# Performance work log

Measured on AMD Instinct MI355X. Metric: run time of the kernel, lower is better.

The kernel has to match this reference:

```python
import jax, jax.numpy as jnp
import numpy as np

B, N, IN_DIM = 64, 4096, 128
D = 128          # slot_size
S = 7            # num_slots
ITERS = 3
HID = 256        # mlp_hdim
EPS = 1e-8       # renorm epsilon
LN_EPS = 1e-5    # torch LayerNorm default


def _ln(x, g, b):
    m = jnp.mean(x, axis=-1, keepdims=True)
    v = jnp.mean((x - m) ** 2, axis=-1, keepdims=True)
    return (x - m) * jax.lax.rsqrt(v + LN_EPS) * g + b


def setup_inputs() -> dict:
    key = jax.random.key(0)
    ks = jax.random.split(key, 16)
    s = 0.02
    return {
        "x": jax.random.normal(ks[0], (B, N, IN_DIM), jnp.float32),
        "noise": jax.random.normal(ks[1], (B, S, D), jnp.float32),
        "Wq": jax.random.normal(ks[2], (D, D), jnp.float32) * s,
        "Wk": jax.random.normal(ks[3], (D, IN_DIM), jnp.float32) * s,
        "Wv": jax.random.normal(ks[4], (D, IN_DIM), jnp.float32) * s,
        "ln_in_g": jnp.ones((IN_DIM,), jnp.float32),
        "ln_in_b": jnp.zeros((IN_DIM,), jnp.float32),
        "ln_slots_g": jnp.ones((D,), jnp.float32),
        "ln_slots_b": jnp.zeros((D,), jnp.float32),
        "ln_mlp_g": jnp.ones((D,), jnp.float32),
        "ln_mlp_b": jnp.zeros((D,), jnp.float32),
        "W_ih": jax.random.normal(ks[5], (3 * D, D), jnp.float32) * s,
        "W_hh": jax.random.normal(ks[6], (3 * D, D), jnp.float32) * s,
        "b_ih": jnp.zeros((3 * D,), jnp.float32),
        "b_hh": jnp.zeros((3 * D,), jnp.float32),
        "W1": jax.random.normal(ks[7], (HID, D), jnp.float32) * s,
        "b1": jnp.zeros((HID,), jnp.float32),
        "W2": jax.random.normal(ks[8], (D, HID), jnp.float32) * s,
        "b2": jnp.zeros((D,), jnp.float32),
        "mu": jax.random.normal(ks[9], (1, 1, D), jnp.float32) * s,
        "logsigma": jax.random.normal(ks[10], (1, D), jnp.float32) * s,
    }


def reference(x, noise, Wq, Wk, Wv, ln_in_g, ln_in_b, ln_slots_g, ln_slots_b,
              ln_mlp_g, ln_mlp_b, W_ih, W_hh, b_ih, b_hh, W1, b1, W2, b2,
              mu, logsigma):
    xn = _ln(x, ln_in_g, ln_in_b)              # (B,N,IN)
    k = xn @ Wk.T                              # (B,N,D)
    v = xn @ Wv.T                              # (B,N,D)

    scale = jax.nn.softplus(logsigma)[None] + 1e-5   # (1,1,D)
    slots = mu + scale * noise                 # rsample, (B,S,D)

    def gru(u, h):
        gx = u @ W_ih.T + b_ih                 # (B*S, 3D)
        gh = h @ W_hh.T + b_hh
        xr, xz, xn_ = jnp.split(gx, 3, axis=-1)
        hr, hz, hn = jnp.split(gh, 3, axis=-1)
        r = jax.nn.sigmoid(xr + hr)
        z = jax.nn.sigmoid(xz + hz)
        n = jnp.tanh(xn_ + r * hn)
        return (1.0 - z) * n + z * h

    inv_sqrt_d = D ** -0.5
    for _ in range(ITERS):
        slots_prev = slots
        sn = _ln(slots, ln_slots_g, ln_slots_b)
        q = sn @ Wq.T                          # (B,S,D)
        scores = inv_sqrt_d * jnp.einsum('bnd,bsd->bns', k, q)
        attn = jax.nn.softmax(scores, axis=-1)           # over slots
        attn = attn + EPS
        attn = attn / jnp.sum(attn, axis=1, keepdims=True)  # renorm over inputs
        updates = jnp.einsum('bns,bnd->bsd', attn, v)    # (B,S,D)
        h = gru(updates.reshape(-1, D), slots_prev.reshape(-1, D))
        slots = h.reshape(x.shape[0], S, D)
        slots = _ln(slots, ln_mlp_g, ln_mlp_b)
        slots = slots + (jax.nn.relu(slots @ W1.T + b1) @ W2.T + b2)
    return slots
```

## Files before the change

kernel.cpp:

```cpp
#include <hip/hip_runtime.h>
#include <hip/hip_bf16.h>
#include <stdint.h>

#define B_ 64
#define N_ 4096
#define D_ 128
#define S_ 7
#define EPS_ 1e-8f
#define LN_EPS_ 1e-5f
#define SC_INV 0.08838834764831843f

typedef float  f32x4  __attribute__((ext_vector_type(4)));
typedef __bf16 bf16x8 __attribute__((ext_vector_type(8)));

#define WIH_OFF 0
#define WHH_OFF 49152
#define W1_OFF  98304
#define W2_OFF  131072
#define WQ_OFF  163840
#define WKT_OFF 180224
#define WV_OFF  196608
#define WBF_TOT 212992

__device__ __forceinline__ uint16_t f2bfbits(float f) {
    uint32_t x = __float_as_uint(f);
    return (uint16_t)((x + 0x7fffu + ((x >> 16) & 1u)) >> 16);
}
__device__ __forceinline__ uint32_t pk2(float a, float b) {
    return (uint32_t)f2bfbits(a) | ((uint32_t)f2bfbits(b) << 16);
}

__global__ __launch_bounds__(256) void k_init_prep(
    const float* __restrict__ noise, const float* __restrict__ Wk,
    const float* __restrict__ mu, const float* __restrict__ logsigma,
    const float* __restrict__ Wq, const float* __restrict__ lsg,
    const float* __restrict__ lsb,
    const float* __restrict__ Wih, const float* __restrict__ Whh,
    const float* __restrict__ W1, const float* __restrict__ W2,
    const float* __restrict__ Wv,
    float* __restrict__ slots, uint16_t* __restrict__ kqbf,
    uint16_t* __restrict__ wbf,
    const float* __restrict__ x, const float* __restrict__ lng,
    const float* __restrict__ lnb, uint16_t* __restrict__ xn) {
    const int t = threadIdx.x;
    if (blockIdx.x < 448) {
        __shared__ float sn[128], qr[128];
        __shared__ float red[2];
        const int tid = blockIdx.x * 256 + t;
        const int row = blockIdx.x;
        const int b = row / 7, s = row - b * 7;
        bool act = t < 128;
        float v = 0.f;
        if (act) {
            float sc = log1pf(__expf(logsigma[t])) + 1e-5f;
            v = mu[t] + sc * noise[row * 128 + t];
            slots[row * 128 + t] = v;
        }
        float sv = act ? v : 0.f;
        #pragma unroll
        for (int m = 1; m < 64; m <<= 1) sv += __shfl_xor(sv, m);
        if (act && (t & 63) == 0) red[t >> 6] = sv;
        __syncthreads();
        float mean = (red[0] + red[1]) * (1.0f / 128.0f);
        __syncthreads();
        float dv = act ? (v - mean) : 0.f;
        float sq = dv * dv;
        #pragma unroll
        for (int m = 1; m < 64; m <<= 1) sq += __shfl_xor(sq, m);
        if (act && (t & 63) == 0) red[t >> 6] = sq;
        __syncthreads();
        float var = (red[0] + red[1]) * (1.0f / 128.0f);
        if (act) sn[t] = dv * rsqrtf(var + LN_EPS_) * lsg[t] + lsb[t];
        __syncthreads();
        if (act) {
            const float4* wr = (const float4*)(Wq + t * 128);
            float acc = 0.f;
            #pragma unroll 8
            for (int j = 0; j < 32; ++j) {
                float4 w = wr[j];
                float4 s4 = *(const float4*)(sn + 4 * j);
                acc += w.x * s4.x + w.y * s4.y + w.z * s4.z + w.w * s4.w;
            }
            qr[t] = acc;
        }
        __syncthreads();
        if (act) {
            float kq = 0.f;
            #pragma unroll 8
            for (int o = 0; o < 128; ++o) kq += qr[o] * Wk[o * 128 + t];
            int elem = (t >> 5) * 512 + (s + 16 * ((t >> 3) & 3)) * 8 + (t & 7);
            kqbf[b * 2048 + elem] = f2bfbits(kq * SC_INV);
        }
        if (tid < 73728) {
            int bb = tid / 1152, rem = tid - bb * 1152;
            int sp = 7 + (rem >> 7), d = rem & 127;
            int elem = (d >> 5) * 512 + (sp + 16 * ((d >> 3) & 3)) * 8 + (d & 7);
            kqbf[bb * 2048 + elem] = 0;
        }
        for (int e = tid; e < WBF_TOT; e += 448 * 256) {
            const float* W; int C, el, mode = 0;
            if (e < WHH_OFF)      { W = Wih; C = 128; el = e; }
            else if (e < W1_OFF)  { W = Whh; C = 128; el = e - WHH_OFF; }
            else if (e < W2_OFF)  { W = W1;  C = 128; el = e - W1_OFF; }
            else if (e < WQ_OFF)  { W = W2;  C = 256; el = e - W2_OFF; }
            else if (e < WKT_OFF) { W = Wq;  C = 128; el = e - WQ_OFF; }
            else if (e < WV_OFF)  { W = Wk;  C = 128; el = e - WKT_OFF; mode = 1; }
            else                  { W = Wv;  C = 128; el = e - WV_OFF; }
            int tile = el >> 9, within = el & 511;
            int lp = within >> 3, j = within & 7;
            int lm_ = lp & 15, qd_ = lp >> 4;
            float w;
            if (!mode) {
                int ktN = C >> 5, ot = tile / ktN, kt = tile - ot * ktN;
                w = W[(ot * 16 + lm_) * C + kt * 32 + qd_ * 8 + j];
            } else {
                int dt = tile >> 2, kt = tile & 3;
                w = W[(kt * 32 + qd_ * 8 + j) * 128 + dt * 16 + lm_];
            }
            wbf[e] = f2bfbits(w);
        }
        return;
    }
    const int pid = blockIdx.x - 448;
    const int wv = t >> 6, lane = t & 63;
    const int lm = lane & 15, hi = lane >> 4;
    const long row = (long)pid * 64 + wv * 16 + lm;
    const long ntile = (long)pid * 4 + wv;
    const float* xp = x + row * 128 + hi * 8;
    f32x4 xa[4][2];
    #pragma unroll
    for (int k0 = 0; k0 < 4; ++k0) {
        xa[k0][0] = *(const f32x4*)(xp + k0 * 32);
        xa[k0][1] = *(const f32x4*)(xp + k0 * 32 + 4);
    }
    float s = 0.f, sq = 0.f;
    #pragma unroll
    for (int k0 = 0; k0 < 4; ++k0)
        #pragma unroll
        for (int c = 0; c < 2; ++c)
            #pragma unroll
            for (int r = 0; r < 4; ++r) { float v = xa[k0][c][r]; s += v; sq += v * v; }
    s  += __shfl_xor(s, 16);  s  += __shfl_xor(s, 32);
    sq += __shfl_xor(sq, 16); sq += __shfl_xor(sq, 32);
    float mean = s * (1.0f / 128.0f);
    float var  = sq * (1.0f / 128.0f) - mean * mean;
    float rs   = rsqrtf(var + LN_EPS_);
    #pragma unroll
    for (int k0 = 0; k0 < 4; ++k0) {
        f32x4 g0 = *(const f32x4*)(lng + k0 * 32 + hi * 8);
        f32x4 g1 = *(const f32x4*)(lng + k0 * 32 + hi * 8 + 4);
        f32x4 b0 = *(const f32x4*)(lnb + k0 * 32 + hi * 8);
        f32x4 b1 = *(const f32x4*)(lnb + k0 * 32 + hi * 8 + 4);
        float v[8];
        #pragma unroll
        for (int r = 0; r < 4; ++r) {
            v[r]     = (xa[k0][0][r] - mean) * rs * g0[r] + b0[r];
            v[4 + r] = (xa[k0][1][r] - mean) * rs * g1[r] + b1[r];
        }
        uint4 st;
        st.x = pk2(v[0], v[1]); st.y = pk2(v[2], v[3]);
        st.z = pk2(v[4], v[5]); st.w = pk2(v[6], v[7]);
        *(uint4*)(xn + (ntile * 4 + k0) * 512 + lane * 8) = st;
    }
}

__global__ __launch_bounds__(256, 4) void k_attn(
    const uint16_t* __restrict__ xn, const uint16_t* __restrict__ kqbf,
    float* __restrict__ upart, float* __restrict__ cpart) {
    __shared__ __align__(16) uint16_t stage[4][32 * 132];
    __shared__ __align__(16) uint16_t als[4][16 * 36];
    __shared__ float bsum[4][8];
    const int t = threadIdx.x, wv = t >> 6, lane = t & 63;
    const int lm = lane & 15, qd = lane >> 4;
    const int b = blockIdx.x >> 4, chunk = blockIdx.x & 15;
    const int ntb = b * 256 + chunk * 16 + wv * 4;
    const int sbase = qd * 4;

    bf16x8 kqf[4];
    #pragma unroll
    for (int k0 = 0; k0 < 4; ++k0)
        kqf[k0] = *(const bf16x8*)(kqbf + b * 2048 + k0 * 512 + lane * 8);

    bf16x8 xfs[2][2][4];
    #pragma unroll
    for (int sub = 0; sub < 2; ++sub)
        #pragma unroll
        for (int nt = 0; nt < 2; ++nt)
            #pragma unroll
            for (int k0 = 0; k0 < 4; ++k0)
                xfs[sub][nt][k0] = *(const bf16x8*)(xn +
                    ((long)(ntb + sub * 2 + nt) * 4 + k0) * 512 + lane * 8);

    uint16_t* xw = stage[wv];
    float* prt = (float*)stage[wv];
    uint16_t* aw = als[wv];
    f32x4 uacc[8];
    #pragma unroll
    for (int i = 0; i < 8; ++i) uacc[i] = (f32x4){0.f, 0.f, 0.f, 0.f};
    f32x4 csl = {0.f, 0.f, 0.f, 0.f};

    #pragma unroll
    for (int sub = 0; sub < 2; ++sub) {
        #pragma unroll
        for (int nt = 0; nt < 2; ++nt)
            #pragma unroll
            for (int k0 = 0; k0 < 4; ++k0) {
                int base = (nt * 16 + lm) * 132 + k0 * 32 + qd * 8;
                const uint2* src = (const uint2*)&xfs[sub][nt][k0];
                *(uint2*)(xw + base)     = src[0];
                *(uint2*)(xw + base + 4) = src[1];
            }
        f32x4 sc[2];
        #pragma unroll
        for (int nt = 0; nt < 2; ++nt) {
            f32x4 acc = {0.f, 0.f, 0.f, 0.f};
            #pragma unroll
            for (int k0 = 0; k0 < 4; ++k0)
                acc = __builtin_amdgcn_mfma_f32_16x16x32_bf16(kqf[k0], xfs[sub][nt][k0], acc, 0, 0, 0);
            sc[nt] = acc;
        }
        #pragma unroll
        for (int nt = 0; nt < 2; ++nt) {
            float mx = -1e30f;
            #pragma unroll
            for (int r = 0; r < 4; ++r)
                if (sbase + r < 7) mx = fmaxf(mx, sc[nt][r]);
            mx = fmaxf(mx, __shfl_xor(mx, 16));
            mx = fmaxf(mx, __shfl_xor(mx, 32));
            float e[4], tot = 0.f;
            #pragma unroll
            for (int r = 0; r < 4; ++r) {
                e[r] = (sbase + r < 7) ? __expf(sc[nt][r] - mx) : 0.f;
                tot += e[r];
            }
            tot += __shfl_xor(tot, 16);
            tot += __shfl_xor(tot, 32);
            float inv = 1.0f / tot;
            #pragma unroll
            for (int r = 0; r < 4; ++r) {
                float a_ = (sbase + r < 7) ? e[r] * inv + EPS_ : 0.f;
                csl[r] += a_;
                aw[(sbase + r) * 36 + nt * 16 + lm] = f2bfbits(a_);
            }
        }
        union { uint2 u[2]; bf16x8 v; } cva;
        cva.u[0] = *(const uint2*)(aw + lm * 36 + qd * 8);
        cva.u[1] = *(const uint2*)(aw + lm * 36 + qd * 8 + 4);
        bf16x8 afr = cva.v;
        #pragma unroll
        for (int dt = 0; dt < 8; ++dt) {
            bf16x8 bfr;
            #pragma unroll
            for (int j = 0; j < 8; ++j)
                bfr[j] = ((const __bf16*)xw)[(qd * 8 + j) * 132 + dt * 16 + lm];
            uacc[dt] = __builtin_amdgcn_mfma_f32_16x16x32_bf16(afr, bfr, uacc[dt], 0, 0, 0);
        }
    }
    #pragma unroll
    for (int m = 1; m < 16; m <<= 1) {
        csl[0] += __shfl_xor(csl[0], m);
        csl[1] += __shfl_xor(csl[1], m);
        csl[2] += __shfl_xor(csl[2], m);
        csl[3] += __shfl_xor(csl[3], m);
    }
    if (lm == 0) {
        #pragma unroll
        for (int r = 0; r < 4; ++r) {
            int s = sbase + r;
            if (s < 7) bsum[wv][s] = csl[r];
        }
    }
    #pragma unroll
    for (int dt = 0; dt < 8; ++dt)
        #pragma unroll
        for (int r = 0; r < 4; ++r) {
            int s = sbase + r;
            if (s < 7) prt[s * 132 + dt * 16 + lm] = uacc[dt][r];
        }
    __syncthreads();
    if (t < 128) {
        const float* p0 = (const float*)stage[0];
        const float* p1 = (const float*)stage[1];
        const float* p2 = (const float*)stage[2];
        const float* p3 = (const float*)stage[3];
        #pragma unroll
        for (int s = 0; s < 7; ++s) {
            int o = s * 132 + t;
            upart[((b * 16 + chunk) * 7 + s) * 128 + t] = p0[o] + p1[o] + p2[o] + p3[o];
        }
    }
    if (t < 7)
        cpart[(b * 16 + chunk) * 7 + t] = bsum[0][t] + bsum[1][t] + bsum[2][t] + bsum[3][t];
}

__global__ __launch_bounds__(256) void k_fused(
    const float* __restrict__ upart, const float* __restrict__ cpart,
    float* __restrict__ slots, const uint16_t* __restrict__ wbf,
    const float* __restrict__ bih, const float* __restrict__ bhh,
    const float* __restrict__ gm, const float* __restrict__ bm,
    const float* __restrict__ b1, const float* __restrict__ b2,
    const float* __restrict__ lsg, const float* __restrict__ lsb,
    uint16_t* __restrict__ kqbf, float* __restrict__ dst, int hasq) {
    __shared__ float uf[16][132];
    __shared__ float hf[16][132];
    __shared__ float slf[16][132];
    __shared__ float hidl[16][264];
    __shared__ float glg[7][776];
    __shared__ float csl[7];
    const int b = blockIdx.x;
    const int t = threadIdx.x, wv = t >> 6, lane = t & 63;
    const int lm = lane & 15, qd = lane >> 4;

    if (t < 7) {
        float c = 0.f;
        #pragma unroll
        for (int i = 0; i < 16; ++i) c += cpart[(b * 16 + i) * 7 + t];
        csl[t] = c;
    }
    for (int idx = t; idx < 896; idx += 256) {
        int s = idx >> 7, d = idx & 127;
        float acc = 0.f;
        #pragma unroll
        for (int i = 0; i < 16; ++i) acc += upart[((b * 16 + i) * 7 + s) * 128 + d];
        slf[s][d] = acc;
        hf[s][d] = slots[(b * 7 + s) * 128 + d];
    }
    __syncthreads();

    {
        bf16x8 apb[4];
        #pragma unroll
        for (int k0 = 0; k0 < 4; ++k0)
            #pragma unroll
            for (int j = 0; j < 8; ++j) apb[k0][j] = (__bf16)slf[lm][k0 * 32 + qd * 8 + j];
        #pragma unroll
        for (int i = 0; i < 2; ++i) {
            int dt = wv * 2 + i;
            f32x4 acc = {0.f, 0.f, 0.f, 0.f};
            #pragma unroll
            for (int k0 = 0; k0 < 4; ++k0) {
                bf16x8 bf = *(const bf16x8*)(wbf + WV_OFF + ((dt * 4 + k0) << 9) + lane * 8);
                acc = __builtin_amdgcn_mfma_f32_16x16x32_bf16(apb[k0], bf, acc, 0, 0, 0);
            }
            #pragma unroll
            for (int r = 0; r < 4; ++r) {
                int s = qd * 4 + r;
                if (s < 7) uf[s][dt * 16 + lm] = acc[r] / csl[s];
            }
        }
    }
    __syncthreads();

    bf16x8 au[4], ah[4];
    #pragma unroll
    for (int k0 = 0; k0 < 4; ++k0)
        #pragma unroll
        for (int j = 0; j < 8; ++j) {
            au[k0][j] = (__bf16)uf[lm][k0 * 32 + qd * 8 + j];
            ah[k0][j] = (__bf16)hf[lm][k0 * 32 + qd * 8 + j];
        }
    {
        const int ih = (wv < 2);
        const uint16_t* W = wbf + (ih ? WIH_OFF : WHH_OFF);
        const int base = ih ? 0 : 384;
        const int w2 = wv & 1;
        #pragma unroll
        for (int i = 0; i < 12; ++i) {
            int ot = w2 * 12 + i;
            f32x4 acc = {0.f, 0.f, 0.f, 0.f};
            #pragma unroll
            for (int k0 = 0; k0 < 4; ++k0) {
                bf16x8 bf = *(const bf16x8*)(W + ((ot * 4 + k0) << 9) + lane * 8);
                acc = __builtin_amdgcn_mfma_f32_16x16x32_bf16(ih ? au[k0] : ah[k0], bf, acc, 0, 0, 0);
            }
            #pragma unroll
            for (int r = 0; r < 4; ++r) {
                int s = qd * 4 + r;
                if (s < 7) glg[s][base + ot * 16 + lm] = acc[r];
            }
        }
    }
    __syncthreads();

    for (int idx = t; idx < 896; idx += 256) {
        int s = idx >> 7, d = idx & 127;
        float xr = glg[s][d] + bih[d];
        float xz = glg[s][128 + d] + bih[128 + d];
        float xg = glg[s][256 + d] + bih[256 + d];
        float hr = glg[s][384 + d] + bhh[d];
        float hz = glg[s][512 + d] + bhh[128 + d];
        float hg = glg[s][640 + d] + bhh[256 + d];
        float r = 1.f / (1.f + __expf(-(xr + hr)));
        float z = 1.f / (1.f + __expf(-(xz + hz)));
        float n = tanhf(xg + r * hg);
        uf[s][d] = (1.f - z) * n + z * hf[s][d];
    }
    __syncthreads();

    for (int s = wv; s < 7; s += 4) {
        float a0 = uf[s][2 * lane], a1 = uf[s][2 * lane + 1];
        float sm = a0 + a1, sq = a0 * a0 + a1 * a1;
        #pragma unroll
        for (int m = 1; m < 64; m <<= 1) { sm += __shfl_xor(sm, m); sq += __shfl_xor(sq, m); }
        float mean = sm * (1.0f / 128.0f);
        float var = sq * (1.0f / 128.0f) - mean * mean;
        float rs = rsqrtf(var + LN_EPS_);
        slf[s][2 * lane]     = (a0 - mean) * rs * gm[2 * lane] + bm[2 * lane];
        slf[s][2 * lane + 1] = (a1 - mean) * rs * gm[2 * lane + 1] + bm[2 * lane + 1];
    }
    __syncthreads();

    bf16x8 as_[4];
    #pragma unroll
    for (int k0 = 0; k0 < 4; ++k0)
        #pragma unroll
        for (int j = 0; j < 8; ++j) as_[k0][j] = (__bf16)slf[lm][k0 * 32 + qd * 8 + j];
    #pragma unroll
    for (int i = 0; i < 4; ++i) {
        int ot = wv * 4 + i;
        f32x4 acc = {0.f, 0.f, 0.f, 0.f};
        #pragma unroll
        for (int k0 = 0; k0 < 4; ++k0) {
            bf16x8 bf = *(const bf16x8*)(wbf + W1_OFF + ((ot * 4 + k0) << 9) + lane * 8);
            acc = __builtin_amdgcn_mfma_f32_16x16x32_bf16(as_[k0], bf, acc, 0, 0, 0);
        }
        #pragma unroll
        for (int r = 0; r < 4; ++r) {
            int s = qd * 4 + r;
            if (s < 7) hidl[s][ot * 16 + lm] = fmaxf(acc[r] + b1[ot * 16 + lm], 0.f);
        }
    }
    __syncthreads();

    bf16x8 ahd[8];
    #pragma unroll
    for (int k0 = 0; k0 < 8; ++k0)
        #pragma unroll
        for (int j = 0; j < 8; ++j) ahd[k0][j] = (__bf16)hidl[lm][k0 * 32 + qd * 8 + j];
    #pragma unroll
    for (int i = 0; i < 2; ++i) {
        int ot = wv * 2 + i;
        f32x4 acc = {0.f, 0.f, 0.f, 0.f};
        #pragma unroll
        for (int k0 = 0; k0 < 8; ++k0) {
            bf16x8 bf = *(const bf16x8*)(wbf + W2_OFF + ((ot * 8 + k0) << 9) + lane * 8);
            acc = __builtin_amdgcn_mfma_f32_16x16x32_bf16(ahd[k0], bf, acc, 0, 0, 0);
        }
        #pragma unroll
        for (int r = 0; r < 4; ++r) {
            int s = qd * 4 + r;
            if (s < 7) {
                float v = slf[s][ot * 16 + lm] + acc[r] + b2[ot * 16 + lm];
                hf[s][ot * 16 + lm] = v;
                dst[(b * 7 + s) * 128 + ot * 16 + lm] = v;
            }
        }
    }
    if (hasq) {
        __syncthreads();
        for (int s = wv; s < 7; s += 4) {
            float a0 = hf[s][2 * lane], a1 = hf[s][2 * lane + 1];
            float sm = a0 + a1, sq = a0 * a0 + a1 * a1;
            #pragma unroll
            for (int m = 1; m < 64; m <<= 1) { sm += __shfl_xor(sm, m); sq += __shfl_xor(sq, m); }
            float mean = sm * (1.0f / 128.0f);
            float var = sq * (1.0f / 128.0f) - mean * mean;
            float rs = rsqrtf(var + LN_EPS_);
            uf[s][2 * lane]     = (a0 - mean) * rs * lsg[2 * lane] + lsb[2 * lane];
            uf[s][2 * lane + 1] = (a1 - mean) * rs * lsg[2 * lane + 1] + lsb[2 * lane + 1];
        }
        __syncthreads();
        bf16x8 an[4];
        #pragma unroll
        for (int k0 = 0; k0 < 4; ++k0)
            #pragma unroll
            for (int j = 0; j < 8; ++j) an[k0][j] = (__bf16)uf[lm][k0 * 32 + qd * 8 + j];
        #pragma unroll
        for (int i = 0; i < 2; ++i) {
            int ot = wv * 2 + i;
            f32x4 acc = {0.f, 0.f, 0.f, 0.f};
            #pragma unroll
            for (int k0 = 0; k0 < 4; ++k0) {
                bf16x8 bf = *(const bf16x8*)(wbf + WQ_OFF + ((ot * 4 + k0) << 9) + lane * 8);
                acc = __builtin_amdgcn_mfma_f32_16x16x32_bf16(an[k0], bf, acc, 0, 0, 0);
            }
            #pragma unroll
            for (int r = 0; r < 4; ++r) {
                int s = qd * 4 + r;
                if (s < 7) slf[s][ot * 16 + lm] = acc[r];
            }
        }
        __syncthreads();
        bf16x8 aq[4];
        #pragma unroll
        for (int k0 = 0; k0 < 4; ++k0)
            #pragma unroll
            for (int j = 0; j < 8; ++j) aq[k0][j] = (__bf16)slf[lm][k0 * 32 + qd * 8 + j];
        #pragma unroll
        for (int i = 0; i < 2; ++i) {
            int dt = wv * 2 + i;
            f32x4 acc = {0.f, 0.f, 0.f, 0.f};
            #pragma unroll
            for (int k0 = 0; k0 < 4; ++k0) {
                bf16x8 bf = *(const bf16x8*)(wbf + WKT_OFF + ((dt * 4 + k0) << 9) + lane * 8);
                acc = __builtin_amdgcn_mfma_f32_16x16x32_bf16(aq[k0], bf, acc, 0, 0, 0);
            }
            #pragma unroll
            for (int r = 0; r < 4; ++r) {
                int s = qd * 4 + r;
                if (s < 7) hidl[s][dt * 16 + lm] = acc[r];
            }
        }
        __syncthreads();
        {
            int kt = t >> 6, lp = t & 63;
            int lmp = lp & 15, qdp = lp >> 4;
            uint16_t h[8];
            #pragma unroll
            for (int j = 0; j < 8; ++j)
                h[j] = (lmp < 7) ? f2bfbits(hidl[lmp][kt * 32 + qdp * 8 + j] * SC_INV) : (uint16_t)0;
            uint4 st;
            st.x = (uint32_t)h[0] | ((uint32_t)h[1] << 16);
            st.y = (uint32_t)h[2] | ((uint32_t)h[3] << 16);
            st.z = (uint32_t)h[4] | ((uint32_t)h[5] << 16);
            st.w = (uint32_t)h[6] | ((uint32_t)h[7] << 16);
            *(uint4*)(kqbf + b * 2048 + t * 8) = st;
        }
    }
}

extern "C" void kernel_launch(void* const* d_in, const int* in_sizes, int n_in,
                              void* d_out, int out_size, void* d_ws, size_t ws_size,
                              hipStream_t stream) {
    const float* x    = (const float*)d_in[0];
    const float* nz   = (const float*)d_in[1];
    const float* Wq   = (const float*)d_in[2];
    const float* Wk   = (const float*)d_in[3];
    const float* Wv   = (const float*)d_in[4];
    const float* ling = (const float*)d_in[5];
    const float* linb = (const float*)d_in[6];
    const float* lsg  = (const float*)d_in[7];
    const float* lsb  = (const float*)d_in[8];
    const float* lmg  = (const float*)d_in[9];
    const float* lmb  = (const float*)d_in[10];
    const float* Wih  = (const float*)d_in[11];
    const float* Whh  = (const float*)d_in[12];
    const float* bih  = (const float*)d_in[13];
    const float* bhh  = (const float*)d_in[14];
    const float* W1   = (const float*)d_in[15];
    const float* b1   = (const float*)d_in[16];
    const float* W2   = (const float*)d_in[17];
    const float* b2   = (const float*)d_in[18];
    const float* mu   = (const float*)d_in[19];
    const float* lsig = (const float*)d_in[20];

    char* wsb = (char*)d_ws;
    uint16_t* xn    = (uint16_t*)(wsb);
    uint16_t* wbf   = (uint16_t*)(wsb + (size_t)67108864);
    uint16_t* kqbf  = (uint16_t*)(wsb + (size_t)67534848);
    float*    slots = (float*)  (wsb + (size_t)67796992);
    float*    upart = (float*)  (wsb + (size_t)68026368);
    float*    cpart = (float*)  (wsb + (size_t)71696384);

    k_init_prep<<<4544, 256, 0, stream>>>(nz, Wk, mu, lsig, Wq, lsg, lsb,
                                          Wih, Whh, W1, W2, Wv, slots, kqbf, wbf,
                                          x, ling, linb, xn);
    for (int it = 0; it < 3; ++it) {
        float* dst = (it == 2) ? (float*)d_out : slots;
        k_attn<<<1024, 256, 0, stream>>>(xn, kqbf, upart, cpart);
        k_fused<<<64, 256, 0, stream>>>(upart, cpart, slots, wbf, bih, bhh,
                                        lmg, lmb, b1, b2, lsg, lsb,
                                        kqbf, dst, (it < 2) ? 1 : 0);
    }
}
```

Before: 351.7 us.

## Double rows per LN-prep block and halve per-block work in attention kernel

The input LayerNorm prep blocks now each process 128 rows (two 64-row groups), which halves that grid. The attention kernel now splits each batch across 32 chunks instead of 16, with each wave handling one 32-row subtile instead of two, so it launches twice as many blocks. The fused kernel reduces 32 partials per batch, and the workspace offset for cpart is moved to fit the larger upart. The aim is more parallelism and latency hiding in the attention pass and fewer blocks in prep, at the cost of more partial-sum traffic and reduction work in k_fused.

After: 356.1 us. No clear change (+1.2%).

```diff
diff --git a/kernel.cpp b/kernel.cpp
--- a/kernel.cpp
+++ b/kernel.cpp
@@ -124,43 +124,56 @@
     const int pid = blockIdx.x - 448;
     const int wv = t >> 6, lane = t & 63;
     const int lm = lane & 15, hi = lane >> 4;
-    const long row = (long)pid * 64 + wv * 16 + lm;
-    const long ntile = (long)pid * 4 + wv;
-    const float* xp = x + row * 128 + hi * 8;
-    f32x4 xa[4][2];
+    const long row0 = (long)pid * 128 + wv * 16 + lm;
+    const long row1 = row0 + 64;
+    const long nt0 = (long)pid * 8 + wv;
+    const long nt1 = nt0 + 4;
+    const float* xp0 = x + row0 * 128 + hi * 8;
+    const float* xp1 = x + row1 * 128 + hi * 8;
+    f32x4 xa[2][4][2];
     #pragma unroll
     for (int k0 = 0; k0 < 4; ++k0) {
-        xa[k0][0] = *(const f32x4*)(xp + k0 * 32);
-        xa[k0][1] = *(const f32x4*)(xp + k0 * 32 + 4);
-    }
-    float s = 0.f, sq = 0.f;
-    #pragma unroll
-    for (int k0 = 0; k0 < 4; ++k0)
-        #pragma unroll
-        for (int c = 0; c < 2; ++c)
-            #pragma unroll
-            for (int r = 0; r < 4; ++r) { float v = xa[k0][c][r]; s += v; sq += v * v; }
-    s  += __shfl_xor(s, 16);  s  += __shfl_xor(s, 32);
-    sq += __shfl_xor(sq, 16); sq += __shfl_xor(sq, 32);
-    float mean = s * (1.0f / 128.0f);
-    float var  = sq * (1.0f / 128.0f) - mean * mean;
-    float rs   = rsqrtf(var + LN_EPS_);
+        xa[0][k0][0] = *(const f32x4*)(xp0 + k0 * 32);
+        xa[0][k0][1] = *(const f32x4*)(xp0 + k0 * 32 + 4);
+        xa[1][k0][0] = *(const f32x4*)(xp1 + k0 * 32);
+        xa[1][k0][1] = *(const f32x4*)(xp1 + k0 * 32 + 4);
+    }
+    float mean[2], rs[2];
+    #pragma unroll
+    for (int g = 0; g < 2; ++g) {
+        float s = 0.f, sq = 0.f;
+        #pragma unroll
+        for (int k0 = 0; k0 < 4; ++k0)
+            #pragma unroll
+            for (int c = 0; c < 2; ++c)
+                #pragma unroll
+                for (int r = 0; r < 4; ++r) { float v = xa[g][k0][c][r]; s += v; sq += v * v; }
+        s  += __shfl_xor(s, 16);  s  += __shfl_xor(s, 32);
+        sq += __shfl_xor(sq, 16); sq += __shfl_xor(sq, 32);
+        mean[g] = s * (1.0f / 128.0f);
+        float var = sq * (1.0f / 128.0f) - mean[g] * mean[g];
+        rs[g] = rsqrtf(var + LN_EPS_);
+    }
     #pragma unroll
     for (int k0 = 0; k0 < 4; ++k0) {
         f32x4 g0 = *(const f32x4*)(lng + k0 * 32 + hi * 8);
         f32x4 g1 = *(const f32x4*)(lng + k0 * 32 + hi * 8 + 4);
         f32x4 b0 = *(const f32x4*)(lnb + k0 * 32 + hi * 8);
         f32x4 b1 = *(const f32x4*)(lnb + k0 * 32 + hi * 8 + 4);
-        float v[8];
-        #pragma unroll
-        for (int r = 0; r < 4; ++r) {
-            v[r]     = (xa[k0][0][r] - mean) * rs * g0[r] + b0[r];
-            v[4 + r] = (xa[k0][1][r] - mean) * rs * g1[r] + b1[r];
-        }
-        uint4 st;
-        st.x = pk2(v[0], v[1]); st.y = pk2(v[2], v[3]);
-        st.z = pk2(v[4], v[5]); st.w = pk2(v[6], v[7]);
-        *(uint4*)(xn + (ntile * 4 + k0) * 512 + lane * 8) = st;
+        #pragma unroll
+        for (int g = 0; g < 2; ++g) {
+            float v[8];
+            #pragma unroll
+            for (int r = 0; r < 4; ++r) {
+                v[r]     = (xa[g][k0][0][r] - mean[g]) * rs[g] * g0[r] + b0[r];
+                v[4 + r] = (xa[g][k0][1][r] - mean[g]) * rs[g] * g1[r] + b1[r];
+            }
+            uint4 st;
+            st.x = pk2(v[0], v[1]); st.y = pk2(v[2], v[3]);
+            st.z = pk2(v[4], v[5]); st.w = pk2(v[6], v[7]);
+            long ntile = (g == 0) ? nt0 : nt1;
+            *(uint4*)(xn + (ntile * 4 + k0) * 512 + lane * 8) = st;
+        }
     }
 }
 
@@ -172,8 +185,8 @@
     __shared__ float bsum[4][8];
     const int t = threadIdx.x, wv = t >> 6, lane = t & 63;
     const int lm = lane & 15, qd = lane >> 4;
-    const int b = blockIdx.x >> 4, chunk = blockIdx.x & 15;
-    const int ntb = b * 256 + chunk * 16 + wv * 4;
+    const int b = blockIdx.x >> 5, chunk = blockIdx.x & 31;
+    const int ntb = b * 256 + chunk * 8 + wv * 2;
     const int sbase = qd * 4;
 
     bf16x8 kqf[4];
@@ -181,15 +194,13 @@
     for (int k0 = 0; k0 < 4; ++k0)
         kqf[k0] = *(const bf16x8*)(kqbf + b * 2048 + k0 * 512 + lane * 8);
 
-    bf16x8 xfs[2][2][4];
-    #pragma unroll
-    for (int sub = 0; sub < 2; ++sub)
-        #pragma unroll
-        for (int nt = 0; nt < 2; ++nt)
-            #pragma unroll
-            for (int k0 = 0; k0 < 4; ++k0)
-                xfs[sub][nt][k0] = *(const bf16x8*)(xn +
-                    ((long)(ntb + sub * 2 + nt) * 4 + k0) * 512 + lane * 8);
+    bf16x8 xfs[2][4];
+    #pragma unroll
+    for (int nt = 0; nt < 2; ++nt)
+        #pragma unroll
+        for (int k0 = 0; k0 < 4; ++k0)
+            xfs[nt][k0] = *(const bf16x8*)(xn +
+                ((long)(ntb + nt) * 4 + k0) * 512 + lane * 8);
 
     uint16_t* xw = stage[wv];
     float* prt = (float*)stage[wv];
@@ -200,61 +211,58 @@
     f32x4 csl = {0.f, 0.f, 0.f, 0.f};
 
     #pragma unroll
-    for (int sub = 0; sub < 2; ++sub) {
-        #pragma unroll
-        for (int nt = 0; nt < 2; ++nt)
-            #pragma unroll
-            for (int k0 = 0; k0 < 4; ++k0) {
-                int base = (nt * 16 + lm) * 132 + k0 * 32 + qd * 8;
-                const uint2* src = (const uint2*)&xfs[sub][nt][k0];
-                *(uint2*)(xw + base)     = src[0];
-                *(uint2*)(xw + base + 4) = src[1];
-            }
-        f32x4 sc[2];
-        #pragma unroll
-        for (int nt = 0; nt < 2; ++nt) {
-            f32x4 acc = {0.f, 0.f, 0.f, 0.f};
-            #pragma unroll
-            for (int k0 = 0; k0 < 4; ++k0)
-                acc = __builtin_amdgcn_mfma_f32_16x16x32_bf16(kqf[k0], xfs[sub][nt][k0], acc, 0, 0, 0);
-            sc[nt] = acc;
-        }
-        #pragma unroll
-        for (int nt = 0; nt < 2; ++nt) {
-            float mx = -1e30f;
-            #pragma unroll
-            for (int r = 0; r < 4; ++r)
-                if (sbase + r < 7) mx = fmaxf(mx, sc[nt][r]);
-            mx = fmaxf(mx, __shfl_xor(mx, 16));
-            mx = fmaxf(mx, __shfl_xor(mx, 32));
-            float e[4], tot = 0.f;
-            #pragma unroll
-            for (int r = 0; r < 4; ++r) {
-                e[r] = (sbase + r < 7) ? __expf(sc[nt][r] - mx) : 0.f;
-                tot += e[r];
-            }
-            tot += __shfl_xor(tot, 16);
-            tot += __shfl_xor(tot, 32);
-            float inv = 1.0f / tot;
-            #pragma unroll
-            for (int r = 0; r < 4; ++r) {
-                float a_ = (sbase + r < 7) ? e[r] * inv + EPS_ : 0.f;
-                csl[r] += a_;
-                aw[(sbase + r) * 36 + nt * 16 + lm] = f2bfbits(a_);
-            }
-        }
-        union { uint2 u[2]; bf16x8 v; } cva;
-        cva.u[0] = *(const uint2*)(aw + lm * 36 + qd * 8);
-        cva.u[1] = *(const uint2*)(aw + lm * 36 + qd * 8 + 4);
-        bf16x8 afr = cva.v;
-        #pragma unroll
-        for (int dt = 0; dt < 8; ++dt) {
-            bf16x8 bfr;
-            #pragma unroll
-            for (int j = 0; j < 8; ++j)
-                bfr[j] = ((const __bf16*)xw)[(qd * 8 + j) * 132 + dt * 16 + lm];
-            uacc[dt] = __builtin_amdgcn_mfma_f32_16x16x32_bf16(afr, bfr, uacc[dt], 0, 0, 0);
-        }
+    for (int nt = 0; nt < 2; ++nt)
+        #pragma unroll
+        for (int k0 = 0; k0 < 4; ++k0) {
+            int base = (nt * 16 + lm) * 132 + k0 * 32 + qd * 8;
+            const uint2* src = (const uint2*)&xfs[nt][k0];
+            *(uint2*)(xw + base)     = src[0];
+            *(uint2*)(xw + base + 4) = src[1];
+        }
+    f32x4 sc[2];
+    #pragma unroll
+    for (int nt = 0; nt < 2; ++nt) {
+        f32x4 acc = {0.f, 0.f, 0.f, 0.f};
+        #pragma unroll
+        for (int k0 = 0; k0 < 4; ++k0)
+            acc = __builtin_amdgcn_mfma_f32_16x16x32_bf16(kqf[k0], xfs[nt][k0], acc, 0, 0, 0);
+        sc[nt] = acc;
+    }
+    #pragma unroll
+    for (int nt = 0; nt < 2; ++nt) {
+        float mx = -1e30f;
+        #pragma unroll
+        for (int r = 0; r < 4; ++r)
+            if (sbase + r < 7) mx = fmaxf(mx, sc[nt][r]);
+        mx = fmaxf(mx, __shfl_xor(mx, 16));
+        mx = fmaxf(mx, __shfl_xor(mx, 32));
+        float e[4], tot = 0.f;
+        #pragma unroll
+        for (int r = 0; r < 4; ++r) {
+            e[r] = (sbase + r < 7) ? __expf(sc[nt][r] - mx) : 0.f;
+            tot += e[r];
+        }
+        tot += __shfl_xor(tot, 16);
+        tot += __shfl_xor(tot, 32);
+        float inv = 1.0f / tot;
+        #pragma unroll
+        for (int r = 0; r < 4; ++r) {
+            float a_ = (sbase + r < 7) ? e[r] * inv + EPS_ : 0.f;
+            csl[r] += a_;
+            aw[(sbase + r) * 36 + nt * 16 + lm] = f2bfbits(a_);
+        }
+    }
+    union { uint2 u[2]; bf16x8 v; } cva;
+    cva.u[0] = *(const uint2*)(aw + lm * 36 + qd * 8);
+    cva.u[1] = *(const uint2*)(aw + lm * 36 + qd * 8 + 4);
+    bf16x8 afr = cva.v;
+    #pragma unroll
+    for (int dt = 0; dt < 8; ++dt) {
+        bf16x8 bfr;
+        #pragma unroll
+        for (int j = 0; j < 8; ++j)
+            bfr[j] = ((const __bf16*)xw)[(qd * 8 + j) * 132 + dt * 16 + lm];
+        uacc[dt] = __builtin_amdgcn_mfma_f32_16x16x32_bf16(afr, bfr, uacc[dt], 0, 0, 0);
     }
     #pragma unroll
     for (int m = 1; m < 16; m <<= 1) {
@@ -286,11 +294,11 @@
         #pragma unroll
         for (int s = 0; s < 7; ++s) {
             int o = s * 132 + t;
-            upart[((b * 16 + chunk) * 7 + s) * 128 + t] = p0[o] + p1[o] + p2[o] + p3[o];
+            upart[((b * 32 + chunk) * 7 + s) * 128 + t] = p0[o] + p1[o] + p2[o] + p3[o];
         }
     }
     if (t < 7)
-        cpart[(b * 16 + chunk) * 7 + t] = bsum[0][t] + bsum[1][t] + bsum[2][t] + bsum[3][t];
+        cpart[(b * 32 + chunk) * 7 + t] = bsum[0][t] + bsum[1][t] + bsum[2][t] + bsum[3][t];
 }
 
 __global__ __launch_bounds__(256) void k_fused(
@@ -314,14 +322,14 @@
     if (t < 7) {
         float c = 0.f;
         #pragma unroll
-        for (int i = 0; i < 16; ++i) c += cpart[(b * 16 + i) * 7 + t];
+        for (int i = 0; i < 32; ++i) c += cpart[(b * 32 + i) * 7 + t];
         csl[t] = c;
     }
     for (int idx = t; idx < 896; idx += 256) {
         int s = idx >> 7, d = idx & 127;
         float acc = 0.f;
         #pragma unroll
-        for (int i = 0; i < 16; ++i) acc += upart[((b * 16 + i) * 7 + s) * 128 + d];
+        for (int i = 0; i < 32; ++i) acc += upart[((b * 32 + i) * 7 + s) * 128 + d];
         slf[s][d] = acc;
         hf[s][d] = slots[(b * 7 + s) * 128 + d];
     }
@@ -560,14 +568,14 @@
     uint16_t* kqbf  = (uint16_t*)(wsb + (size_t)67534848);
     float*    slots = (float*)  (wsb + (size_t)67796992);
     float*    upart = (float*)  (wsb + (size_t)68026368);
-    float*    cpart = (float*)  (wsb + (size_t)71696384);
-
-    k_init_prep<<<4544, 256, 0, stream>>>(nz, Wk, mu, lsig, Wq, lsg, lsb,
+    float*    cpart = (float*)  (wsb + (size_t)75366400);
+
+    k_init_prep<<<2496, 256, 0, stream>>>(nz, Wk, mu, lsig, Wq, lsg, lsb,
                                           Wih, Whh, W1, W2, Wv, slots, kqbf, wbf,
                                           x, ling, linb, xn);
     for (int it = 0; it < 3; ++it) {
         float* dst = (it == 2) ? (float*)d_out : slots;
-        k_attn<<<1024, 256, 0, stream>>>(xn, kqbf, upart, cpart);
+        k_attn<<<2048, 256, 0, stream>>>(xn, kqbf, upart, cpart);
         k_fused<<<64, 256, 0, stream>>>(upart, cpart, slots, wbf, bih, bhh,
                                         lmg, lmb, b1, b2, lsg, lsb,
                                         kqbf, dst, (it < 2) ? 1 : 0);
```
